# Kernel tuning notes

Hardware: AMD Instinct MI355X
Metric: run time of the kernel (lower is better)

## Reference

```python
import jax, jax.numpy as jnp
import numpy as np

D_MODEL = 1024
NHEAD = 16
D_K = D_MODEL // NHEAD


def setup_inputs() -> dict:
    key = jax.random.key(0)
    ks = jax.random.split(key, 11)
    B, S = 2, 2048
    scale = 1.0 / np.sqrt(D_MODEL)
    inp = {
        "q": jax.random.normal(ks[0], (B, S, D_MODEL), jnp.float32),
        "k": jax.random.normal(ks[1], (B, S, D_MODEL), jnp.float32),
        "v": jax.random.normal(ks[2], (B, S, D_MODEL), jnp.float32),
        "Wq": jax.random.normal(ks[3], (D_MODEL, D_MODEL), jnp.float32) * scale,
        "bq": jnp.zeros((D_MODEL,), jnp.float32),
        "Wk": jax.random.normal(ks[4], (D_MODEL, D_MODEL), jnp.float32) * scale,
        "bk": jnp.zeros((D_MODEL,), jnp.float32),
        "Wv": jax.random.normal(ks[5], (D_MODEL, D_MODEL), jnp.float32) * scale,
        "bv": jnp.zeros((D_MODEL,), jnp.float32),
        "Wo": jax.random.normal(ks[6], (D_MODEL, D_MODEL), jnp.float32) * scale,
        "bo": jnp.zeros((D_MODEL,), jnp.float32),
    }
    return inp


def reference(q, k, v, Wq, bq, Wk, bk, Wv, bv, Wo, bo):
    B, S, _ = q.shape
    # Linear projections (torch Linear: x @ W.T + b), split into heads
    def proj(x, W, b):
        y = jnp.einsum('bsd,ed->bse', x, W) + b
        return y.reshape(B, -1, NHEAD, D_K).transpose(0, 2, 1, 3)  # [B,H,S,Dk]

    qh = proj(q, Wq, bq)
    kh = proj(k, Wk, bk)
    vh = proj(v, Wv, bv)

    scores = jnp.einsum('bhqd,bhkd->bhqk', qh, kh) / jnp.sqrt(
        jnp.asarray(D_K, qh.dtype))
    attn = jax.nn.softmax(scores, axis=-1)  # dropout is identity in eval
    out = jnp.einsum('bhqk,bhkd->bhqd', attn, vh)
    out = out.transpose(0, 2, 1, 3).reshape(B, S, D_MODEL)
    return jnp.einsum('bsd,ed->bse', out, Wo) + bo
```

## Files before the change

kernel.cpp:

```cpp
#include <hip/hip_runtime.h>
#include <stdint.h>
#include <stddef.h>

#define D_MODEL 1024
#define NHEAD   16
#define DK      64
#define BB      2
#define SS      2048
#define NTOK    (BB*SS)

#define SCALE_Q 0.18033688011f

typedef short  short8 __attribute__((ext_vector_type(8)));
typedef __bf16 bf16x8 __attribute__((ext_vector_type(8)));
typedef float  f32x4  __attribute__((ext_vector_type(4)));

__device__ __forceinline__ unsigned short f2bf(float x){
  unsigned int u = __builtin_bit_cast(unsigned int, x);
  u += 0x7fffu + ((u >> 16) & 1u);
  return (unsigned short)(u >> 16);
}

__device__ __forceinline__ unsigned int pack_bf2(float x, float y){
  unsigned int a = __builtin_bit_cast(unsigned int, x) + 0x8000u;
  unsigned int b = __builtin_bit_cast(unsigned int, y) + 0x8000u;
  return __builtin_amdgcn_perm(b, a, 0x07060302u);
}

__device__ __forceinline__ unsigned int cvt_pk_bf16(float lo, float hi){
  unsigned int r;
  asm("v_cvt_pk_bf16_f32 %0, %1, %2" : "=v"(r) : "v"(lo), "v"(hi));
  return r;
}

__device__ __forceinline__ float fast_exp2(float x){
#if __has_builtin(__builtin_amdgcn_exp2f)
  return __builtin_amdgcn_exp2f(x);
#else
  return exp2f(x);
#endif
}

__device__ __forceinline__ f32x4 mfma16(bf16x8 a, bf16x8 b, f32x4 c){
  return __builtin_amdgcn_mfma_f32_16x16x32_bf16(a, b, c, 0, 0, 0);
}

__device__ __forceinline__ void async16(const void* g, void* lds){
  __builtin_amdgcn_global_load_lds(
      (const __attribute__((address_space(1))) unsigned int*)g,
      (__attribute__((address_space(3))) unsigned int*)lds,
      16, 0, 0);
}

__global__ __launch_bounds__(256) void cast_bf16_all(
    const float* __restrict__ q,  const float* __restrict__ k,  const float* __restrict__ v,
    const float* __restrict__ wq, const float* __restrict__ wk, const float* __restrict__ wv,
    const float* __restrict__ wo,
    unsigned short* __restrict__ qb,  unsigned short* __restrict__ kb,  unsigned short* __restrict__ vb,
    unsigned short* __restrict__ wqb, unsigned short* __restrict__ wkb, unsigned short* __restrict__ wvb,
    unsigned short* __restrict__ wob)
{
  const float* src; unsigned short* dst; int n;
  switch (blockIdx.y){
    case 0: src = q;  dst = qb;  n = NTOK*D_MODEL;    break;
    case 1: src = k;  dst = kb;  n = NTOK*D_MODEL;    break;
    case 2: src = v;  dst = vb;  n = NTOK*D_MODEL;    break;
    case 3: src = wq; dst = wqb; n = D_MODEL*D_MODEL; break;
    case 4: src = wk; dst = wkb; n = D_MODEL*D_MODEL; break;
    case 5: src = wv; dst = wvb; n = D_MODEL*D_MODEL; break;
    default: src = wo; dst = wob; n = D_MODEL*D_MODEL; break;
  }
  int i = (blockIdx.x * 256 + threadIdx.x) * 8;
  if (i >= n) return;
  float4 a = *(const float4*)(src + i);
  float4 b = *(const float4*)(src + i + 4);
  short8 o;
  o[0] = (short)f2bf(a.x); o[1] = (short)f2bf(a.y);
  o[2] = (short)f2bf(a.z); o[3] = (short)f2bf(a.w);
  o[4] = (short)f2bf(b.x); o[5] = (short)f2bf(b.y);
  o[6] = (short)f2bf(b.z); o[7] = (short)f2bf(b.w);
  *(short8*)(dst + i) = o;
}

__global__ __launch_bounds__(256) void qkv_gemm(
    const unsigned short* __restrict__ qb, const unsigned short* __restrict__ kb,
    const unsigned short* __restrict__ vb,
    const unsigned short* __restrict__ wqb, const unsigned short* __restrict__ wkb,
    const unsigned short* __restrict__ wvb,
    const float* __restrict__ bq, const float* __restrict__ bk, const float* __restrict__ bv,
    unsigned short* __restrict__ Qh, unsigned short* __restrict__ Kh, unsigned short* __restrict__ Vt)
{
  __shared__ __align__(16) unsigned short S[128*128];
  unsigned short* As = S;
  unsigned short* Bs = S + 128*64;
  const int id = blockIdx.x, z = id >> 8, r = id & 255;
  const unsigned short *A, *Bt; const float* bias; unsigned short* C;
  int bm, bn, N, brow; float scale;
  if (z == 0){ A = qb;  Bt = wqb; bias = bq; C = Qh; bm = (r>>3)*128; bn = (r&7)*128; N = 1024; brow = 0; scale = SCALE_Q; }
  else if (z == 1){ A = kb;  Bt = wkb; bias = bk; C = Kh; bm = (r>>3)*128; bn = (r&7)*128; N = 1024; brow = 0; scale = 1.0f; }
  else            { A = wvb; Bt = vb;  bias = bv; C = Vt; bm = (r&7)*128; bn = (r>>3)*128; N = 4096; brow = 1; scale = 1.0f; }
  const int K = 1024;
  const int tid  = threadIdx.x, lane = tid & 63, w = tid >> 6;
  const int quad = lane >> 4,   l16  = lane & 15;
  const int wm = w >> 1, wn = w & 1;
  const int sw = l16 & 7;
  f32x4 acc[4][4] = {};
  for (int kb_ = 0; kb_ < 16; ++kb_){
    const int k0 = kb_ << 6;
    __syncthreads();
    #pragma unroll
    for (int c = 0; c < 4; ++c){
      int chunk = (w*4 + c)*64 + lane;
      int row = chunk >> 3, c8 = chunk & 7;
      int cs = (c8 ^ (row & 7)) << 3;
      async16(A  + (size_t)(bm + row)*K + k0 + cs, (char*)As + (w*4 + c)*1024);
      async16(Bt + (size_t)(bn + row)*K + k0 + cs, (char*)Bs + (w*4 + c)*1024);
    }
    __syncthreads();
    bf16x8 af[4][2], bf[4][2];
    #pragma unroll
    for (int mt = 0; mt < 4; ++mt)
      #pragma unroll
      for (int ks = 0; ks < 2; ++ks){
        int off = (((ks*4 + quad) ^ sw) << 3);
        af[mt][ks] = *(const bf16x8*)&As[(wm*64 + mt*16 + l16)*64 + off];
        bf[mt][ks] = *(const bf16x8*)&Bs[(wn*64 + mt*16 + l16)*64 + off];
      }
    #pragma unroll
    for (int ks = 0; ks < 2; ++ks)
      #pragma unroll
      for (int mt = 0; mt < 4; ++mt)
        #pragma unroll
        for (int nt = 0; nt < 4; ++nt)
          acc[mt][nt] = mfma16(bf[nt][ks], af[mt][ks], acc[mt][nt]);
  }

  __syncthreads();
  #pragma unroll
  for (int nt = 0; nt < 4; ++nt){
    int nl = wn*64 + nt*16 + 4*quad;
    float4 b4;
    if (!brow) b4 = *(const float4*)&bias[bn + nl];
    #pragma unroll
    for (int mt = 0; mt < 4; ++mt){
      int ml = wm*64 + mt*16 + l16;
      float bmv = brow ? bias[bm + ml] : 0.0f;
      float v0 = (acc[mt][nt][0] + (brow ? bmv : b4.x)) * scale;
      float v1 = (acc[mt][nt][1] + (brow ? bmv : b4.y)) * scale;
      float v2 = (acc[mt][nt][2] + (brow ? bmv : b4.z)) * scale;
      float v3 = (acc[mt][nt][3] + (brow ? bmv : b4.w)) * scale;
      uint2 p; p.x = pack_bf2(v0, v1); p.y = pack_bf2(v2, v3);
      int gl = nl >> 2;
      if (brow){
        int g3 = gl & 7;
        gl = (gl & ~7) | ((g3 & 3)*2 + (g3 >> 2));
      }
      int gs = gl ^ (ml & 14);
      *(uint2*)&S[ml*128 + gs*4] = p;
    }
  }
  __syncthreads();
  {
    int rr_ = tid >> 1, hf = tid & 1;
    size_t rowbase = (size_t)(bm + rr_) * N + bn;
    #pragma unroll
    for (int i = 0; i < 8; ++i){
      int gg = hf*16 + i*2;
      uint4 d = *(const uint4*)&S[rr_*128 + ((gg ^ (rr_ & 14)) << 2)];
      *(uint4*)&C[rowbase + gg*4] = d;
    }
  }
}

__global__ __launch_bounds__(256) void gemm_out(
    const unsigned short* __restrict__ A, const unsigned short* __restrict__ Bt,
    const float* __restrict__ bias, float* __restrict__ C)
{
  __shared__ __align__(16) unsigned short As[64*64];
  __shared__ __align__(16) unsigned short Bs[128*64];
  const int K = 1024, N = 1024;
  const int tid  = threadIdx.x, lane = tid & 63, w = tid >> 6;
  const int quad = lane >> 4,   l16  = lane & 15;
  const int bm = blockIdx.y * 64, bn = blockIdx.x * 128;
  const int sw = l16 & 7;
  f32x4 acc[4][2] = {};
  for (int kb_ = 0; kb_ < 16; ++kb_){
    const int k0 = kb_ << 6;
    __syncthreads();
    #pragma unroll
    for (int c = 0; c < 2; ++c){
      int chunk = (w*2 + c)*64 + lane;
      int row = chunk >> 3, c8 = chunk & 7;
      async16(A + (size_t)(bm + row)*K + k0 + ((c8 ^ (row & 7)) << 3),
              (char*)As + (w*2 + c)*1024);
    }
    #pragma unroll
    for (int c = 0; c < 4; ++c){
      int chunk = (w*4 + c)*64 + lane;
      int row = chunk >> 3, c8 = chunk & 7;
      async16(Bt + (size_t)(bn + row)*K + k0 + ((c8 ^ (row & 7)) << 3),
              (char*)Bs + (w*4 + c)*1024);
    }
    __syncthreads();
    bf16x8 af[4][2], bf[2][2];
    #pragma unroll
    for (int mt = 0; mt < 4; ++mt)
      #pragma unroll
      for (int ks = 0; ks < 2; ++ks)
        af[mt][ks] = *(const bf16x8*)&As[(mt*16 + l16)*64 + (((ks*4 + quad) ^ sw) << 3)];
    #pragma unroll
    for (int nt = 0; nt < 2; ++nt)
      #pragma unroll
      for (int ks = 0; ks < 2; ++ks)
        bf[nt][ks] = *(const bf16x8*)&Bs[(w*32 + nt*16 + l16)*64 + (((ks*4 + quad) ^ sw) << 3)];
    #pragma unroll
    for (int ks = 0; ks < 2; ++ks)
      #pragma unroll
      for (int mt = 0; mt < 4; ++mt)
        #pragma unroll
        for (int nt = 0; nt < 2; ++nt)
          acc[mt][nt] = mfma16(af[mt][ks], bf[nt][ks], acc[mt][nt]);
  }
  #pragma unroll
  for (int mt = 0; mt < 4; ++mt){
    #pragma unroll
    for (int nt = 0; nt < 2; ++nt){
      int col = bn + w*32 + nt*16 + l16;
      float bc = bias[col];
      #pragma unroll
      for (int rr = 0; rr < 4; ++rr){
        int row = bm + mt*16 + quad*4 + rr;
        C[(size_t)row*N + col] = acc[mt][nt][rr] + bc;
      }
    }
  }
}

__global__ __launch_bounds__(256) void attn(
    const unsigned short* __restrict__ Qh, const unsigned short* __restrict__ Kh,
    const unsigned short* __restrict__ Vt, unsigned short* __restrict__ ctx)
{
  __shared__ __align__(16) unsigned short Kbuf[2][64*64];
  __shared__ __align__(16) unsigned short Vbuf[2][64*64];
  __shared__ __align__(16) unsigned short QP[128*64];

  const int tid  = threadIdx.x, lane = tid & 63, w = tid >> 6;
  const int quad = lane >> 4,   l16  = lane & 15;
  const int b = blockIdx.y >> 4, h = blockIdx.y & 15;
  const int q0 = blockIdx.x * 128;
  const int sw = l16 & 7;

  #pragma unroll
  for (int c = 0; c < 4; ++c){
    int s = (w*4 + c)*64 + lane;
    int row = s >> 3, c8 = s & 7;
    async16(Qh + (size_t)(b*SS + q0 + row)*D_MODEL + h*DK + ((c8 ^ (row & 7)) << 3),
            (char*)QP + (w*4 + c)*1024);
  }

  const unsigned short* Kp = Kh + (size_t)(b*SS)*D_MODEL + h*DK;
  const unsigned short* Vp = Vt + (size_t)(h*DK)*NTOK + b*SS;
  const unsigned short* ksrc[2];
  const unsigned short* vsrc[2];
  #pragma unroll
  for (int c = 0; c < 2; ++c){
    int s = (w*2 + c)*64 + lane;
    int row = s >> 3, c8 = s & 7;
    int cs = (c8 ^ (row & 7)) << 3;
    ksrc[c] = Kp + (size_t)row*D_MODEL + cs;
    vsrc[c] = Vp + (size_t)row*NTOK  + cs;
  }

  #pragma unroll
  for (int c = 0; c < 2; ++c){
    async16(ksrc[c], (char*)Kbuf[0] + (w*2 + c)*1024);
    async16(vsrc[c], (char*)Vbuf[0] + (w*2 + c)*1024);
    ksrc[c] += 64*D_MODEL;
    vsrc[c] += 64;
  }
  __syncthreads();

  bf16x8 bq0[2], bq1[2];
  #pragma unroll
  for (int ks = 0; ks < 2; ++ks){
    bq0[ks] = *(const bf16x8*)&QP[(w*32 +      l16)*64 + (((ks*4 + quad) ^ sw) << 3)];
    bq1[ks] = *(const bf16x8*)&QP[(w*32 + 16 + l16)*64 + (((ks*4 + quad) ^ sw) << 3)];
  }

  f32x4 acc[2][4] = {};
  float l0a = 0.0f, l0b = 0.0f, l1a = 0.0f, l1b = 0.0f;

  for (int it = 0; it < 32; ++it){
    const int cur = it & 1;
    #pragma unroll
    for (int c = 0; c < 2; ++c){
      async16(ksrc[c], (char*)Kbuf[1 - cur] + (w*2 + c)*1024);
      async16(vsrc[c], (char*)Vbuf[1 - cur] + (w*2 + c)*1024);
      ksrc[c] += 64*D_MODEL;
      vsrc[c] += 64;
    }
    asm volatile("s_waitcnt vmcnt(4)\n\ts_barrier" ::: "memory");

    const unsigned short* Kc = Kbuf[cur];
    const unsigned short* Vc = Vbuf[cur];

    bf16x8 kf[4][2];
    #pragma unroll
    for (int mt = 0; mt < 4; ++mt)
      #pragma unroll
      for (int ks = 0; ks < 2; ++ks)
        kf[mt][ks] = *(const bf16x8*)&Kc[(mt*16 + l16)*64 + (((ks*4 + quad) ^ sw) << 3)];

    bf16x8 vf[4][2];
    #pragma unroll
    for (int nt = 0; nt < 4; ++nt)
      #pragma unroll
      for (int ks = 0; ks < 2; ++ks)
        vf[nt][ks] = *(const bf16x8*)&Vc[(nt*16 + l16)*64 + (((ks*4 + quad) ^ sw) << 3)];

    f32x4 s0[4] = {}, s1[4] = {};
    #pragma unroll
    for (int mt = 0; mt < 4; ++mt)
      #pragma unroll
      for (int ks = 0; ks < 2; ++ks){
        s0[mt] = mfma16(kf[mt][ks], bq0[ks], s0[mt]);
        s1[mt] = mfma16(kf[mt][ks], bq1[ks], s1[mt]);
      }

    float s0a = 0.0f, s0b = 0.0f, s1a = 0.0f, s1b = 0.0f;
    #pragma unroll
    for (int mt = 0; mt < 4; ++mt)
      #pragma unroll
      for (int rr = 0; rr < 4; ++rr){
        float p0 = fast_exp2(s0[mt][rr]); s0[mt][rr] = p0;
        float p1 = fast_exp2(s1[mt][rr]); s1[mt][rr] = p1;
        if (mt & 1){ s0b += p0; s1b += p1; } else { s0a += p0; s1a += p1; }
      }
    l0a += s0a; l0b += s0b; l1a += s1a; l1b += s1b;

    bf16x8 bp0[2], bp1[2];
    #pragma unroll
    for (int ks = 0; ks < 2; ++ks){
      uint4 t;
      t.x = cvt_pk_bf16(s0[2*ks  ][0], s0[2*ks  ][1]);
      t.y = cvt_pk_bf16(s0[2*ks  ][2], s0[2*ks  ][3]);
      t.z = cvt_pk_bf16(s0[2*ks+1][0], s0[2*ks+1][1]);
      t.w = cvt_pk_bf16(s0[2*ks+1][2], s0[2*ks+1][3]);
      bp0[ks] = __builtin_bit_cast(bf16x8, t);
      t.x = cvt_pk_bf16(s1[2*ks  ][0], s1[2*ks  ][1]);
      t.y = cvt_pk_bf16(s1[2*ks  ][2], s1[2*ks  ][3]);
      t.z = cvt_pk_bf16(s1[2*ks+1][0], s1[2*ks+1][1]);
      t.w = cvt_pk_bf16(s1[2*ks+1][2], s1[2*ks+1][3]);
      bp1[ks] = __builtin_bit_cast(bf16x8, t);
    }

    #pragma unroll
    for (int nt = 0; nt < 4; ++nt)
      #pragma unroll
      for (int ks = 0; ks < 2; ++ks){
        acc[0][nt] = mfma16(vf[nt][ks], bp0[ks], acc[0][nt]);
        acc[1][nt] = mfma16(vf[nt][ks], bp1[ks], acc[1][nt]);
      }

    asm volatile("s_waitcnt lgkmcnt(0)\n\ts_barrier" ::: "memory");
  }

  float l_i[2] = { l0a + l0b, l1a + l1b };
  float inv[2];
  #pragma unroll
  for (int qg = 0; qg < 2; ++qg){
    float t = l_i[qg];
    t += __shfl_xor(t, 16);
    t += __shfl_xor(t, 32);
    inv[qg] = 1.0f / t;
  }
  #pragma unroll
  for (int qg = 0; qg < 2; ++qg){
    int pr = (w*32 + qg*16 + l16)*64;
    #pragma unroll
    for (int nt = 0; nt < 4; ++nt){
      int c8  = nt*2 + (quad >> 1);
      int off = ((c8 ^ sw) << 3) + (quad & 1)*4;
      uint2 p;
      p.x = pack_bf2(acc[qg][nt][0]*inv[qg], acc[qg][nt][1]*inv[qg]);
      p.y = pack_bf2(acc[qg][nt][2]*inv[qg], acc[qg][nt][3]*inv[qg]);
      *(uint2*)&QP[pr + off] = p;
    }
  }
  asm volatile("s_waitcnt lgkmcnt(0)" ::: "memory");
  {
    int r  = w*32 + (lane >> 1);
    int j0 = (lane & 1)*4;
    unsigned short* dst = ctx + (size_t)(b*SS + q0 + r)*D_MODEL + h*DK;
    #pragma unroll
    for (int i = 0; i < 4; ++i){
      int j = j0 + i;
      uint4 d = *(const uint4*)&QP[r*64 + ((j ^ (r & 7)) << 3)];
      *(uint4*)(dst + j*8) = d;
    }
  }
}

extern "C" void kernel_launch(void* const* d_in, const int* in_sizes, int n_in,
                              void* d_out, int out_size, void* d_ws, size_t ws_size,
                              hipStream_t stream) {
  const float* q  = (const float*)d_in[0];
  const float* k  = (const float*)d_in[1];
  const float* v  = (const float*)d_in[2];
  const float* Wq = (const float*)d_in[3];
  const float* bq = (const float*)d_in[4];
  const float* Wk = (const float*)d_in[5];
  const float* bk = (const float*)d_in[6];
  const float* Wv = (const float*)d_in[7];
  const float* bv = (const float*)d_in[8];
  const float* Wo = (const float*)d_in[9];
  const float* bo = (const float*)d_in[10];

  char* ws = (char*)d_ws;
  const size_t TOKB = (size_t)NTOK * D_MODEL * 2;
  const size_t WB   = (size_t)D_MODEL * D_MODEL * 2;
  unsigned short* qb  = (unsigned short*)ws;             ws += TOKB;
  unsigned short* kb  = (unsigned short*)ws;             ws += TOKB;
  unsigned short* vb  = (unsigned short*)ws;             ws += TOKB;
  unsigned short* wqb = (unsigned short*)ws;             ws += WB;
  unsigned short* wkb = (unsigned short*)ws;             ws += WB;
  unsigned short* wvb = (unsigned short*)ws;             ws += WB;
  unsigned short* wob = (unsigned short*)ws;             ws += WB;
  unsigned short* Qh  = (unsigned short*)ws;             ws += TOKB;
  unsigned short* Kh  = (unsigned short*)ws;             ws += TOKB;
  unsigned short* Vt  = (unsigned short*)ws;             ws += TOKB;
  unsigned short* ctx = (unsigned short*)ws;             ws += TOKB;

  cast_bf16_all<<<dim3(2048, 7), 256, 0, stream>>>(q, k, v, Wq, Wk, Wv, Wo,
                                                   qb, kb, vb, wqb, wkb, wvb, wob);
  qkv_gemm<<<dim3(768), 256, 0, stream>>>(qb, kb, vb, wqb, wkb, wvb,
                                          bq, bk, bv, Qh, Kh, Vt);
  attn<<<dim3(SS/128, BB*NHEAD), 256, 0, stream>>>(Qh, Kh, Vt, ctx);
  gemm_out<<<dim3(8, 64), 256, 0, stream>>>(ctx, wob, bo, (float*)d_out);
}
```

Baseline: 232.4 us.

## Double-buffer QKV GEMM K-tiles with async prefetch and remap block order

Splits the shared-memory tile into two 32-wide K buffers so the global-to-LDS load of the next K slice overlaps MFMA work on the current one, using explicit vmcnt waits and barriers in place of the two syncthreads per iteration. The swizzle is adapted to the narrower 32-column rows. Block IDs are also permuted to interleave tiles across workgroups, likely to improve cache locality. The cost is twice as many loop iterations with smaller MFMA bursts, plus hand-written waitcnt logic that must be exactly right. The final iteration issues a prefetch past the end of K, which reads beyond the row and may be out of bounds on the last rows.

```diff
diff --git a/kernel.cpp b/kernel.cpp
--- a/kernel.cpp
+++ b/kernel.cpp
@@ -91,9 +91,14 @@
     unsigned short* __restrict__ Qh, unsigned short* __restrict__ Kh, unsigned short* __restrict__ Vt)
 {
   __shared__ __align__(16) unsigned short S[128*128];
-  unsigned short* As = S;
-  unsigned short* Bs = S + 128*64;
-  const int id = blockIdx.x, z = id >> 8, r = id & 255;
+  unsigned short* As0 = S;
+  unsigned short* Bs0 = S + 4096;
+  unsigned short* As1 = S + 8192;
+  unsigned short* Bs1 = S + 12288;
+
+  int bid = blockIdx.x;
+  const int id = (bid & 7) * 96 + (bid >> 3);
+  const int z = id >> 8, r = id & 255;
   const unsigned short *A, *Bt; const float* bias; unsigned short* C;
   int bm, bn, N, brow; float scale;
   if (z == 0){ A = qb;  Bt = wqb; bias = bq; C = Qh; bm = (r>>3)*128; bn = (r&7)*128; N = 1024; brow = 0; scale = SCALE_Q; }
@@ -103,39 +108,57 @@
   const int tid  = threadIdx.x, lane = tid & 63, w = tid >> 6;
   const int quad = lane >> 4,   l16  = lane & 15;
   const int wm = w >> 1, wn = w & 1;
-  const int sw = l16 & 7;
+  const int fsl = (quad ^ ((l16 >> 2) & 3)) << 3;
+
+  const unsigned short* asrc[2];
+  const unsigned short* bsrc[2];
+  #pragma unroll
+  for (int c = 0; c < 2; ++c){
+    int s = (w*2 + c)*64 + lane;
+    int row = s >> 2, c4 = s & 3;
+    int cs = (c4 ^ ((row >> 2) & 3)) << 3;
+    asrc[c] = A  + (size_t)(bm + row)*K + cs;
+    bsrc[c] = Bt + (size_t)(bn + row)*K + cs;
+  }
+
+  #pragma unroll
+  for (int c = 0; c < 2; ++c){
+    async16(asrc[c], (char*)As0 + (w*2 + c)*1024);
+    async16(bsrc[c], (char*)Bs0 + (w*2 + c)*1024);
+    asrc[c] += 32; bsrc[c] += 32;
+  }
+
   f32x4 acc[4][4] = {};
-  for (int kb_ = 0; kb_ < 16; ++kb_){
-    const int k0 = kb_ << 6;
-    __syncthreads();
-    #pragma unroll
-    for (int c = 0; c < 4; ++c){
-      int chunk = (w*4 + c)*64 + lane;
-      int row = chunk >> 3, c8 = chunk & 7;
-      int cs = (c8 ^ (row & 7)) << 3;
-      async16(A  + (size_t)(bm + row)*K + k0 + cs, (char*)As + (w*4 + c)*1024);
-      async16(Bt + (size_t)(bn + row)*K + k0 + cs, (char*)Bs + (w*4 + c)*1024);
-    }
-    __syncthreads();
-    bf16x8 af[4][2], bf[4][2];
+  for (int t = 0; t < 32; ++t){
+    const int cur = t & 1;
+    unsigned short* An = cur ? As0 : As1;
+    unsigned short* Bn = cur ? Bs0 : Bs1;
+    #pragma unroll
+    for (int c = 0; c < 2; ++c){
+      async16(asrc[c], (char*)An + (w*2 + c)*1024);
+      async16(bsrc[c], (char*)Bn + (w*2 + c)*1024);
+      asrc[c] += 32; bsrc[c] += 32;
+    }
+    asm volatile("s_waitcnt vmcnt(4)\n\ts_barrier" ::: "memory");
+
+    const unsigned short* Ac = cur ? As1 : As0;
+    const unsigned short* Bc = cur ? Bs1 : Bs0;
+    bf16x8 af[4], bf[4];
+    #pragma unroll
+    for (int mt = 0; mt < 4; ++mt){
+      af[mt] = *(const bf16x8*)&Ac[(wm*64 + mt*16 + l16)*32 + fsl];
+      bf[mt] = *(const bf16x8*)&Bc[(wn*64 + mt*16 + l16)*32 + fsl];
+    }
     #pragma unroll
     for (int mt = 0; mt < 4; ++mt)
       #pragma unroll
-      for (int ks = 0; ks < 2; ++ks){
-        int off = (((ks*4 + quad) ^ sw) << 3);
-        af[mt][ks] = *(const bf16x8*)&As[(wm*64 + mt*16 + l16)*64 + off];
-        bf[mt][ks] = *(const bf16x8*)&Bs[(wn*64 + mt*16 + l16)*64 + off];
-      }
-    #pragma unroll
-    for (int ks = 0; ks < 2; ++ks)
-      #pragma unroll
-      for (int mt = 0; mt < 4; ++mt)
-        #pragma unroll
-        for (int nt = 0; nt < 4; ++nt)
-          acc[mt][nt] = mfma16(bf[nt][ks], af[mt][ks], acc[mt][nt]);
-  }
-
-  __syncthreads();
+      for (int nt = 0; nt < 4; ++nt)
+        acc[mt][nt] = mfma16(bf[nt], af[mt], acc[mt][nt]);
+
+    asm volatile("s_waitcnt lgkmcnt(0)\n\ts_barrier" ::: "memory");
+  }
+  asm volatile("s_waitcnt vmcnt(0)\n\ts_barrier" ::: "memory");
+
   #pragma unroll
   for (int nt = 0; nt < 4; ++nt){
     int nl = wn*64 + nt*16 + 4*quad;
```

New measurement: 220.4 us. 5.1% less time.
